# Performance work log

Measured on AMD Instinct MI355X. Metric: run time of the kernel, lower is better.

Reference implementation:

```python
import jax, jax.numpy as jnp
import numpy as np

B, T, C = 64, 384, 256
NH, NKV = 4, 2
HD = C // NH            # 64
NREP = NH // NKV        # 2
NE, TOPK = 8, 2
HID = int(8 / 3 * C)    # 682
EPS_RMS = 1e-6


def _rope_tables(t_len):
    inv_freq = 1.0 / (10000.0 ** (np.arange(0, HD, 2, dtype=np.float32) / HD))
    t = np.arange(t_len, dtype=np.float32)
    freqs = np.outer(t, inv_freq)                      # [T, HD/2]
    emb = np.concatenate([freqs, freqs], axis=-1)      # [T, HD]
    return jnp.asarray(np.cos(emb)), jnp.asarray(np.sin(emb))


def _rotate_half(x):
    h = x.shape[-1] // 2
    return jnp.concatenate([-x[..., h:], x[..., :h]], axis=-1)


def _rmsnorm(v, w):
    return v * jax.lax.rsqrt(jnp.mean(v * v, axis=-1, keepdims=True) + EPS_RMS) * w


def setup_inputs() -> dict:
    key = jax.random.key(0)
    ks = jax.random.split(key, 10)
    s = lambda k, shape: (jax.random.normal(k, shape, jnp.float32) * 0.02)
    return {
        "x": jax.random.normal(ks[0], (B, T, C), jnp.float32),
        "ln1_w": jnp.ones((C,), jnp.float32),
        "ln2_w": jnp.ones((C,), jnp.float32),
        "wq": s(ks[1], (NH * HD, C)),
        "wk": s(ks[2], (NKV * HD, C)),
        "wv": s(ks[3], (NKV * HD, C)),
        "wo": s(ks[4], (C, C)),
        "router_w": s(ks[5], (NE, C)),
        "w1": s(ks[6], (NE, HID, C)),
        "w2": s(ks[7], (NE, C, HID)),
        "w3": s(ks[8], (NE, HID, C)),
    }


def reference(x, ln1_w, ln2_w, wq, wk, wv, wo, router_w, w1, w2, w3):
    Bx, Tx, Cx = x.shape
    # --- attention sub-block ---
    h = _rmsnorm(x, ln1_w)
    q = (h @ wq.T).reshape(Bx, Tx, NH, HD).transpose(0, 2, 1, 3)    # [B,H,T,D]
    k = (h @ wk.T).reshape(Bx, Tx, NKV, HD).transpose(0, 2, 1, 3)   # [B,KV,T,D]
    v = (h @ wv.T).reshape(Bx, Tx, NKV, HD).transpose(0, 2, 1, 3)
    cos, sin = _rope_tables(Tx)
    cos, sin = cos[None, None], sin[None, None]
    q = q * cos + _rotate_half(q) * sin
    k = k * cos + _rotate_half(k) * sin
    k = jnp.repeat(k, NREP, axis=1)   # GQA: expand kv heads
    v = jnp.repeat(v, NREP, axis=1)
    scores = jnp.einsum('bhtd,bhsd->bhts', q, k) / jnp.sqrt(jnp.float32(HD))
    causal = jnp.tril(jnp.ones((Tx, Tx), dtype=bool))
    scores = jnp.where(causal[None, None], scores, jnp.float32(-1e30))
    att = jax.nn.softmax(scores, axis=-1)
    y = jnp.einsum('bhts,bhsd->bhtd', att, v).transpose(0, 2, 1, 3).reshape(Bx, Tx, Cx)
    x = x + y @ wo.T

    # --- MoE sub-block ---
    flat = _rmsnorm(x, ln2_w).reshape(-1, Cx)                  # [N, C]
    probs = jax.nn.softmax(flat @ router_w.T, axis=-1)         # [N, NE]
    tp, ti = jax.lax.top_k(probs, TOPK)
    tp = tp / (jnp.sum(tp, axis=-1, keepdims=True) + 1e-9)
    # per-token per-expert combine weight (0 if not selected)
    weights = jnp.sum(tp[..., None] * jax.nn.one_hot(ti, NE, dtype=flat.dtype), axis=1)  # [N, NE]
    out = jnp.zeros_like(flat)
    for e in range(NE):  # small fixed expert count
        hh = jax.nn.silu(flat @ w1[e].T) * (flat @ w3[e].T)
        out = out + weights[:, e:e + 1] * (hh @ w2[e].T)
    return x + out.reshape(Bx, Tx, Cx)
```

## Files before the change

### kernel.cpp

```cpp
#include <hip/hip_runtime.h>
#include <hip/hip_bf16.h>
#include <math.h>

typedef unsigned short u16t;
typedef __bf16 bf16x8 __attribute__((ext_vector_type(8)));
typedef float f32x4 __attribute__((ext_vector_type(4)));

#define NBATCH 64
#define NT 384
#define NC 256
#define NHID 682
#define NHIDP 704
#define NTOK (NBATCH * NT)
#define NSLOT (2 * NTOK + 1024)

static __device__ __forceinline__ float bf2f(u16t u) { return __uint_as_float(((unsigned int)u) << 16); }
static __device__ __forceinline__ u16t f2bf(float f) { return __builtin_bit_cast(u16t, __float2bfloat16(f)); }

static __device__ __forceinline__ void gload16(const void* gp, void* lp) {
  __builtin_amdgcn_global_load_lds((const __attribute__((address_space(1))) void*)gp,
                                   (__attribute__((address_space(3))) void*)lp, 16, 0, 0);
}


__global__ void k_cvt(const float* __restrict__ src, u16t* __restrict__ dst, int n) {
  int i = blockIdx.x * 256 + threadIdx.x;
  if (i < n) dst[i] = f2bf(src[i]);
}

__global__ __launch_bounds__(256) void k_rms(const float* __restrict__ xin,
                                             const float* __restrict__ wg,
                                             u16t* __restrict__ out) {
  int w = threadIdx.x >> 6, l = threadIdx.x & 63;
  int n = blockIdx.x * 4 + w;
  const float* xr = xin + (size_t)n * NC;
  float4 xa = *(const float4*)(xr + l * 4);
  float ssq = xa.x * xa.x + xa.y * xa.y + xa.z * xa.z + xa.w * xa.w;
  for (int d = 1; d < 64; d <<= 1) ssq += __shfl_xor(ssq, d, 64);
  float rs = rsqrtf(ssq * (1.f / 256.f) + 1e-6f);
  float4 wa = *(const float4*)(wg + l * 4);
  ushort4 o;
  o.x = f2bf(xa.x * rs * wa.x);
  o.y = f2bf(xa.y * rs * wa.y);
  o.z = f2bf(xa.z * rs * wa.z);
  o.w = f2bf(xa.w * rs * wa.w);
  *(ushort4*)(out + (size_t)n * NC + l * 4) = o;
}

__global__ __launch_bounds__(256) void k_rms_router(const float* __restrict__ xin,
                                                    const float* __restrict__ wg,
                                                    const float* __restrict__ rw,
                                                    u16t* __restrict__ flat,
                                                    int* __restrict__ eidx,
                                                    float* __restrict__ ew) {
  int w = threadIdx.x >> 6, l = threadIdx.x & 63;
  int n = blockIdx.x * 4 + w;
  const float* xr = xin + (size_t)n * NC;
  float4 xa = *(const float4*)(xr + l * 4);
  float ssq = xa.x * xa.x + xa.y * xa.y + xa.z * xa.z + xa.w * xa.w;
  for (int d = 1; d < 64; d <<= 1) ssq += __shfl_xor(ssq, d, 64);
  float rs = rsqrtf(ssq * (1.f / 256.f) + 1e-6f);
  float4 wa = *(const float4*)(wg + l * 4);
  float n0 = xa.x * rs * wa.x, n1 = xa.y * rs * wa.y;
  float n2 = xa.z * rs * wa.z, n3 = xa.w * rs * wa.w;
  ushort4 o; o.x = f2bf(n0); o.y = f2bf(n1); o.z = f2bf(n2); o.w = f2bf(n3);
  *(ushort4*)(flat + (size_t)n * NC + l * 4) = o;
  float acc[8];
  for (int e = 0; e < 8; e++) {
    float4 ra = *(const float4*)(rw + (size_t)e * NC + l * 4);
    acc[e] = n0 * ra.x + n1 * ra.y + n2 * ra.z + n3 * ra.w;
  }
  for (int e = 0; e < 8; e++)
    for (int d = 1; d < 64; d <<= 1) acc[e] += __shfl_xor(acc[e], d, 64);
  if (l == 0) {
    float mx = acc[0];
    for (int e = 1; e < 8; e++) mx = fmaxf(mx, acc[e]);
    float p[8], sum = 0.f;
    for (int e = 0; e < 8; e++) { p[e] = __expf(acc[e] - mx); sum += p[e]; }
    float inv = 1.f / sum;
    for (int e = 0; e < 8; e++) p[e] *= inv;
    int i0 = 0; float b0 = p[0];
    for (int e = 1; e < 8; e++) if (p[e] > b0) { b0 = p[e]; i0 = e; }
    int i1 = -1; float b1 = -1.f;
    for (int e = 0; e < 8; e++) if (e != i0 && p[e] > b1) { b1 = p[e]; i1 = e; }
    float s2 = 1.f / (b0 + b1 + 1e-9f);
    eidx[n * 2] = i0; eidx[n * 2 + 1] = i1;
    ew[n * 2] = b0 * s2; ew[n * 2 + 1] = b1 * s2;
  }
}

__global__ __launch_bounds__(256) void k_hist(const int* __restrict__ eidx, int* __restrict__ cnt) {
  __shared__ int lh[8];
  if (threadIdx.x < 8) lh[threadIdx.x] = 0;
  __syncthreads();
  int base = blockIdx.x * 1024 + threadIdx.x;
  for (int i = 0; i < 4; i++) atomicAdd(&lh[eidx[base + i * 256]], 1);
  __syncthreads();
  if (threadIdx.x < 8) atomicAdd(&cnt[threadIdx.x], lh[threadIdx.x]);
}

__global__ __launch_bounds__(256) void k_gemm_bt(const u16t* __restrict__ A,
                                                 const u16t* __restrict__ Bw,
                                                 u16t* __restrict__ Co, int K, int N) {
  __shared__ __align__(16) u16t sA[128 * 64];
  __shared__ __align__(16) u16t sB[128 * 64];
  int t = threadIdx.x;
  int m0 = blockIdx.y * 128, n0 = blockIdx.x * 128;
  int w = t >> 6, l = t & 63, quad = l >> 4, lq = l & 15;
  int wm = (w >> 1) * 64, wn = (w & 1) * 64;
  const f32x4 fz = {0.f, 0.f, 0.f, 0.f};
  f32x4 acc[4][4];
  for (int i = 0; i < 4; i++) for (int j = 0; j < 4; j++) acc[i][j] = fz;
  int nk = K >> 6;
  for (int kb = 0; kb < nk; kb++) {
    int k0 = kb << 6;
    for (int i = 0; i < 4; i++) {
      int c = i * 256 + t; int r = c >> 3; int g = (c & 7) ^ (r & 7);
      gload16(A + (size_t)(m0 + r) * K + k0 + g * 8, sA + (size_t)c * 8);
      gload16(Bw + (size_t)(n0 + r) * K + k0 + g * 8, sB + (size_t)c * 8);
    }
    __syncthreads();
    for (int kk = 0; kk < 2; kk++) {
      int gq = kk * 4 + quad;
      bf16x8 af[4], bf[4];
      for (int mi = 0; mi < 4; mi++) { int row = wm + mi * 16 + lq; af[mi] = *(const bf16x8*)(sA + (row * 8 + (gq ^ (row & 7))) * 8); }
      for (int ni = 0; ni < 4; ni++) { int row = wn + ni * 16 + lq; bf[ni] = *(const bf16x8*)(sB + (row * 8 + (gq ^ (row & 7))) * 8); }
      for (int mi = 0; mi < 4; mi++)
        for (int ni = 0; ni < 4; ni++)
          acc[mi][ni] = __builtin_amdgcn_mfma_f32_16x16x32_bf16(af[mi], bf[ni], acc[mi][ni], 0, 0, 0);
    }
    __syncthreads();
  }
  for (int mi = 0; mi < 4; mi++)
    for (int ni = 0; ni < 4; ni++) {
      int gn = n0 + wn + ni * 16 + lq;
      for (int r = 0; r < 4; r++) {
        int gm = m0 + wm + mi * 16 + quad * 4 + r;
        Co[(size_t)gm * N + gn] = f2bf(acc[mi][ni][r]);
      }
    }
}

__global__ __launch_bounds__(256) void k_gemm_wo(const u16t* __restrict__ A,
                                                 const u16t* __restrict__ Bw,
                                                 const float* __restrict__ xin,
                                                 float* __restrict__ xo) {
  __shared__ __align__(16) u16t sA[128 * 64];
  __shared__ __align__(16) u16t sB[128 * 64];
  int t = threadIdx.x;
  int m0 = blockIdx.y * 128, n0 = blockIdx.x * 128;
  int w = t >> 6, l = t & 63, quad = l >> 4, lq = l & 15;
  int wm = (w >> 1) * 64, wn = (w & 1) * 64;
  const f32x4 fz = {0.f, 0.f, 0.f, 0.f};
  f32x4 acc[4][4];
  for (int i = 0; i < 4; i++) for (int j = 0; j < 4; j++) acc[i][j] = fz;
  for (int kb = 0; kb < 4; kb++) {
    int k0 = kb << 6;
    for (int i = 0; i < 4; i++) {
      int c = i * 256 + t; int r = c >> 3; int g = (c & 7) ^ (r & 7);
      gload16(A + (size_t)(m0 + r) * NC + k0 + g * 8, sA + (size_t)c * 8);
      gload16(Bw + (size_t)(n0 + r) * NC + k0 + g * 8, sB + (size_t)c * 8);
    }
    __syncthreads();
    for (int kk = 0; kk < 2; kk++) {
      int gq = kk * 4 + quad;
      bf16x8 af[4], bf[4];
      for (int mi = 0; mi < 4; mi++) { int row = wm + mi * 16 + lq; af[mi] = *(const bf16x8*)(sA + (row * 8 + (gq ^ (row & 7))) * 8); }
      for (int ni = 0; ni < 4; ni++) { int row = wn + ni * 16 + lq; bf[ni] = *(const bf16x8*)(sB + (row * 8 + (gq ^ (row & 7))) * 8); }
      for (int mi = 0; mi < 4; mi++)
        for (int ni = 0; ni < 4; ni++)
          acc[mi][ni] = __builtin_amdgcn_mfma_f32_16x16x32_bf16(af[mi], bf[ni], acc[mi][ni], 0, 0, 0);
    }
    __syncthreads();
  }
  for (int mi = 0; mi < 4; mi++)
    for (int ni = 0; ni < 4; ni++) {
      int gn = n0 + wn + ni * 16 + lq;
      for (int r = 0; r < 4; r++) {
        int gm = m0 + wm + mi * 16 + quad * 4 + r;
        xo[(size_t)gm * NC + gn] = acc[mi][ni][r] + xin[(size_t)gm * NC + gn];
      }
    }
}

__global__ __launch_bounds__(192) void k_rope(u16t* __restrict__ q, u16t* __restrict__ kbuf) {
  int n = blockIdx.x; int t = n % NT;
  int i = threadIdx.x;
  u16t* base; int d;
  if (i < 128) { base = q + (size_t)n * NC + (i >> 5) * 64; d = i & 31; }
  else { int j = i - 128; base = kbuf + (size_t)n * 128 + (j >> 5) * 64; d = j & 31; }
  float x1 = bf2f(base[d]), x2 = bf2f(base[d + 32]);
  float ang = (float)t * powf(10000.f, -(float)d * (1.f / 32.f));
  float s, c; sincosf(ang, &s, &c);
  base[d] = f2bf(x1 * c - x2 * s);
  base[d + 32] = f2bf(x2 * c + x1 * s);
}

__global__ __launch_bounds__(256) void k_attn(const u16t* __restrict__ q,
                                              const u16t* __restrict__ kbuf,
                                              const u16t* __restrict__ vbuf,
                                              u16t* __restrict__ y) {
  __shared__ __align__(16) u16t sK[64 * 64];
  __shared__ __align__(16) u16t sVT[64 * 64];
  __shared__ __align__(16) u16t sP[4 * 32 * 64];
  int qt = blockIdx.x, h = blockIdx.y, b = blockIdx.z;
  int kvh = h >> 1;
  int t = threadIdx.x, w = t >> 6, l = t & 63, quad = l >> 4, lq = l & 15;
  int tb = qt * 128 + w * 32;
  bf16x8 qf[2][2];
  for (int mi = 0; mi < 2; mi++)
    for (int kk = 0; kk < 2; kk++)
      qf[mi][kk] = *(const bf16x8*)(q + ((size_t)(b * NT + tb + mi * 16 + lq)) * NC + h * 64 + kk * 32 + quad * 8);
  const f32x4 fz = {0.f, 0.f, 0.f, 0.f};
  f32x4 accO[2][4];
  float mrow[2][4], lrow[2][4];
  for (int mi = 0; mi < 2; mi++)
    for (int ni = 0; ni < 4; ni++) accO[mi][ni] = fz;
  for (int mi = 0; mi < 2; mi++)
    for (int r = 0; r < 4; r++) { mrow[mi][r] = -1e30f; lrow[mi][r] = 0.f; }
  u16t* myP = sP + w * 2048;
  int nkt = (qt + 1) * 2;
  for (int kt = 0; kt < nkt; kt++) {
    int s0 = kt * 64;
    for (int i = 0; i < 2; i++) {
      int c = i * 256 + t; int s = c >> 3; int g = (c & 7) ^ (s & 7);
      gload16(kbuf + ((size_t)(b * NT + s0 + s)) * 128 + kvh * 64 + g * 8, sK + (size_t)c * 8);
    }
    for (int i = 0; i < 2; i++) {
      int p = i * 256 + t; int n0g = p >> 6; int s = p & 63; int n0 = n0g * 8;
      const u16t* vp = vbuf + ((size_t)(b * NT + s0 + s)) * 128 + kvh * 64 + n0;
      ushort4 v0 = *(const ushort4*)vp; ushort4 v1 = *(const ushort4*)(vp + 4);
      u16t vv[8] = {v0.x, v0.y, v0.z, v0.w, v1.x, v1.y, v1.z, v1.w};
      for (int j = 0; j < 8; j++) {
        int nn = n0 + j;
        sVT[(nn * 8 + ((s >> 3) ^ (nn & 7))) * 8 + (s & 7)] = vv[j];
      }
    }
    __syncthreads();
    if (s0 <= tb + 31) {
      f32x4 accS[2][4];
      for (int mi = 0; mi < 2; mi++) for (int ni = 0; ni < 4; ni++) accS[mi][ni] = fz;
      for (int kk = 0; kk < 2; kk++) {
        int gq = kk * 4 + quad;
        bf16x8 kf[4];
        for (int ni = 0; ni < 4; ni++) { int row = ni * 16 + lq; kf[ni] = *(const bf16x8*)(sK + (row * 8 + (gq ^ (row & 7))) * 8); }
        for (int mi = 0; mi < 2; mi++)
          for (int ni = 0; ni < 4; ni++)
            accS[mi][ni] = __builtin_amdgcn_mfma_f32_16x16x32_bf16(qf[mi][kk], kf[ni], accS[mi][ni], 0, 0, 0);
      }
      for (int mi = 0; mi < 2; mi++) {
        float alpha[4];
        for (int r = 0; r < 4; r++) {
          int trow = tb + mi * 16 + quad * 4 + r;
          float mx = -1e30f;
          for (int ni = 0; ni < 4; ni++) {
            int ss = s0 + ni * 16 + lq;
            float sv = accS[mi][ni][r] * 0.125f;
            sv = (ss > trow) ? -1e30f : sv;
            accS[mi][ni][r] = sv;
            mx = fmaxf(mx, sv);
          }
          for (int d = 1; d < 16; d <<= 1) mx = fmaxf(mx, __shfl_xor(mx, d, 64));
          float mnew = fmaxf(mrow[mi][r], mx);
          float al = __expf(mrow[mi][r] - mnew);
          float rsum = 0.f;
          for (int ni = 0; ni < 4; ni++) {
            float p = __expf(accS[mi][ni][r] - mnew);
            accS[mi][ni][r] = p;
            rsum += p;
          }
          for (int d = 1; d < 16; d <<= 1) rsum += __shfl_xor(rsum, d, 64);
          lrow[mi][r] = lrow[mi][r] * al + rsum;
          mrow[mi][r] = mnew;
          alpha[r] = al;
        }
        for (int ni = 0; ni < 4; ni++)
          for (int r = 0; r < 4; r++) accO[mi][ni][r] *= alpha[r];
        for (int ni = 0; ni < 4; ni++) {
          int cc = ni * 16 + lq;
          for (int r = 0; r < 4; r++) {
            int row = mi * 16 + quad * 4 + r;
            myP[((cc >> 3) * 32 + row) * 8 + (cc & 7)] = f2bf(accS[mi][ni][r]);
          }
        }
      }
      asm volatile("s_waitcnt lgkmcnt(0)" ::: "memory");
      for (int kk = 0; kk < 2; kk++) {
        int gq = kk * 4 + quad;
        bf16x8 pf[2], vf[4];
        for (int mi = 0; mi < 2; mi++) { int row = mi * 16 + lq; pf[mi] = *(const bf16x8*)(myP + (gq * 32 + row) * 8); }
        for (int ni = 0; ni < 4; ni++) { int row = ni * 16 + lq; vf[ni] = *(const bf16x8*)(sVT + (row * 8 + (gq ^ (row & 7))) * 8); }
        for (int mi = 0; mi < 2; mi++)
          for (int ni = 0; ni < 4; ni++)
            accO[mi][ni] = __builtin_amdgcn_mfma_f32_16x16x32_bf16(pf[mi], vf[ni], accO[mi][ni], 0, 0, 0);
      }
    }
    __syncthreads();
  }
  for (int mi = 0; mi < 2; mi++)
    for (int r = 0; r < 4; r++) {
      int trow = tb + mi * 16 + quad * 4 + r;
      float inv = 1.f / lrow[mi][r];
      for (int ni = 0; ni < 4; ni++) {
        int d = ni * 16 + lq;
        y[((size_t)(b * NT + trow)) * NC + h * 64 + d] = f2bf(accO[mi][ni][r] * inv);
      }
    }
}

__global__ void k_init(int* __restrict__ tok, float* __restrict__ tokw, int* __restrict__ ctrl) {
  int i = blockIdx.x * 256 + threadIdx.x;
  if (i < NSLOT) { tok[i] = -1; tokw[i] = 0.f; }
  if (blockIdx.x == 0 && threadIdx.x < 64) ctrl[threadIdx.x] = 0;
}

__global__ void k_scan(const int* __restrict__ cnt, int* __restrict__ offs, int* __restrict__ cursor) {
  if (threadIdx.x == 0) {
    int off = 0;
    for (int e = 0; e < 8; e++) {
      offs[e] = off; cursor[e] = off;
      off += ((cnt[e] + 127) >> 7) << 7;
    }
    offs[8] = off;
  }
}

__global__ __launch_bounds__(256) void k_scatter(const int* __restrict__ eidx, const float* __restrict__ ew,
                                                 int* __restrict__ cursor, int* __restrict__ tok,
                                                 float* __restrict__ tokw, int* __restrict__ t2s) {
  __shared__ int lcnt[8], lbase[8];
  if (threadIdx.x < 8) lcnt[threadIdx.x] = 0;
  __syncthreads();
  int n = blockIdx.x * 256 + threadIdx.x;
  int e0 = eidx[n * 2], e1 = eidx[n * 2 + 1];
  int p0 = atomicAdd(&lcnt[e0], 1);
  int p1 = atomicAdd(&lcnt[e1], 1);
  __syncthreads();
  if (threadIdx.x < 8) lbase[threadIdx.x] = atomicAdd(&cursor[threadIdx.x], lcnt[threadIdx.x]);
  __syncthreads();
  int g0 = lbase[e0] + p0, g1 = lbase[e1] + p1;
  tok[g0] = n; tokw[g0] = ew[n * 2];
  tok[g1] = n; tokw[g1] = ew[n * 2 + 1];
  t2s[n * 2] = g0; t2s[n * 2 + 1] = g1;
}

__global__ void k_pack13(const float* __restrict__ w1, const float* __restrict__ w3,
                         u16t* __restrict__ w1p, u16t* __restrict__ w3p) {
  int idx = blockIdx.x * 256 + threadIdx.x;
  int kcol = idx & 255; int tmp = idx >> 8; int nrow = tmp % NHIDP; int e = tmp / NHIDP;
  if (nrow < NHID) {
    size_t src = ((size_t)e * NHID + nrow) * NC + kcol;
    w1p[idx] = f2bf(w1[src]); w3p[idx] = f2bf(w3[src]);
  } else { w1p[idx] = 0; w3p[idx] = 0; }
}

__global__ void k_pack2(const float* __restrict__ w2, u16t* __restrict__ w2p) {
  int idx = blockIdx.x * 256 + threadIdx.x;
  int kcol = idx % NHIDP; int tmp = idx / NHIDP; int nrow = tmp & 255; int e = tmp >> 8;
  w2p[idx] = (kcol < NHID) ? f2bf(w2[((size_t)e * NC + nrow) * NHID + kcol]) : (u16t)0;
}

__global__ __launch_bounds__(256) void k_moe_e1(const u16t* __restrict__ flat,
                                                const u16t* __restrict__ w1p,
                                                const u16t* __restrict__ w3p,
                                                const int* __restrict__ offs,
                                                const int* __restrict__ tok,
                                                u16t* __restrict__ hh) {
  __shared__ __align__(16) u16t sA[128 * 64];
  __shared__ __align__(16) u16t sB1[64 * 64];
  __shared__ __align__(16) u16t sB3[64 * 64];
  int t = threadIdx.x;
  int bid = blockIdx.x;
  int work = (bid & 7) * 539 + (bid >> 3);
  int sb = work / 11;
  int slot0 = sb * 128, n0 = (work - sb * 11) * 64;
  int e = 7;
  for (int i = 0; i < 8; i++) { if (slot0 < offs[i + 1]) { e = i; break; } }
  const u16t* B1 = w1p + (size_t)e * NHIDP * NC;
  const u16t* B3 = w3p + (size_t)e * NHIDP * NC;
  int w = t >> 6, l = t & 63, quad = l >> 4, lq = l & 15;
  int wm = (w >> 1) * 64, wn = (w & 1) * 32;
  const f32x4 fz = {0.f, 0.f, 0.f, 0.f};
  f32x4 a1[4][2], a3[4][2];
  for (int i = 0; i < 4; i++) for (int j = 0; j < 2; j++) { a1[i][j] = fz; a3[i][j] = fz; }
  for (int kb = 0; kb < 4; kb++) {
    int k0 = kb << 6;
    for (int i = 0; i < 4; i++) {
      int c = i * 256 + t; int r = c >> 3; int g = (c & 7) ^ (r & 7);
      int tk = tok[slot0 + r]; int row = (tk < 0) ? 0 : tk;
      gload16(flat + (size_t)row * NC + k0 + g * 8, sA + (size_t)c * 8);
    }
    for (int i = 0; i < 2; i++) {
      int c = i * 256 + t; int r = c >> 3; int g = (c & 7) ^ (r & 7);
      gload16(B1 + (size_t)(n0 + r) * NC + k0 + g * 8, sB1 + (size_t)c * 8);
      gload16(B3 + (size_t)(n0 + r) * NC + k0 + g * 8, sB3 + (size_t)c * 8);
    }
    __syncthreads();
    for (int kk = 0; kk < 2; kk++) {
      int gq = kk * 4 + quad;
      bf16x8 af[4], b1f[2], b3f[2];
      for (int mi = 0; mi < 4; mi++) { int row = wm + mi * 16 + lq; af[mi] = *(const bf16x8*)(sA + (row * 8 + (gq ^ (row & 7))) * 8); }
      for (int ni = 0; ni < 2; ni++) {
        int row = wn + ni * 16 + lq;
        b1f[ni] = *(const bf16x8*)(sB1 + (row * 8 + (gq ^ (row & 7))) * 8);
        b3f[ni] = *(const bf16x8*)(sB3 + (row * 8 + (gq ^ (row & 7))) * 8);
      }
      for (int mi = 0; mi < 4; mi++)
        for (int ni = 0; ni < 2; ni++) {
          a1[mi][ni] = __builtin_amdgcn_mfma_f32_16x16x32_bf16(af[mi], b1f[ni], a1[mi][ni], 0, 0, 0);
          a3[mi][ni] = __builtin_amdgcn_mfma_f32_16x16x32_bf16(af[mi], b3f[ni], a3[mi][ni], 0, 0, 0);
        }
    }
    __syncthreads();
  }
  for (int mi = 0; mi < 4; mi++)
    for (int ni = 0; ni < 2; ni++) {
      int gn = n0 + wn + ni * 16 + lq;
      for (int r = 0; r < 4; r++) {
        int slot = slot0 + wm + mi * 16 + quad * 4 + r;
        float v1 = a1[mi][ni][r], v3 = a3[mi][ni][r];
        float hv = v1 / (1.f + __expf(-v1)) * v3;
        hh[(size_t)slot * NHIDP + gn] = f2bf(hv);
      }
    }
}

__global__ __launch_bounds__(256) void k_moe_e2(const u16t* __restrict__ hh,
                                                const u16t* __restrict__ w2p,
                                                const int* __restrict__ offs,
                                                const float* __restrict__ tokw,
                                                u16t* __restrict__ eo) {
  __shared__ __align__(16) u16t sA[128 * 64];
  __shared__ __align__(16) u16t sB[128 * 64];
  int t = threadIdx.x;
  int bid = blockIdx.x;
  int work = (bid & 7) * 98 + (bid >> 3);
  int slot0 = (work >> 1) * 128, n0 = (work & 1) * 128;
  int e = 7;
  for (int i = 0; i < 8; i++) { if (slot0 < offs[i + 1]) { e = i; break; } }
  const u16t* Bw = w2p + (size_t)e * NC * NHIDP;
  int w = t >> 6, l = t & 63, quad = l >> 4, lq = l & 15;
  int wm = (w >> 1) * 64, wn = (w & 1) * 64;
  const f32x4 fz = {0.f, 0.f, 0.f, 0.f};
  f32x4 acc[4][4];
  for (int i = 0; i < 4; i++) for (int j = 0; j < 4; j++) acc[i][j] = fz;
  for (int kb = 0; kb < 11; kb++) {
    int k0 = kb << 6;
    for (int i = 0; i < 4; i++) {
      int c = i * 256 + t; int r = c >> 3; int g = (c & 7) ^ (r & 7);
      gload16(hh + (size_t)(slot0 + r) * NHIDP + k0 + g * 8, sA + (size_t)c * 8);
      gload16(Bw + (size_t)(n0 + r) * NHIDP + k0 + g * 8, sB + (size_t)c * 8);
    }
    __syncthreads();
    for (int kk = 0; kk < 2; kk++) {
      int gq = kk * 4 + quad;
      bf16x8 af[4], bf[4];
      for (int mi = 0; mi < 4; mi++) { int row = wm + mi * 16 + lq; af[mi] = *(const bf16x8*)(sA + (row * 8 + (gq ^ (row & 7))) * 8); }
      for (int ni = 0; ni < 4; ni++) { int row = wn + ni * 16 + lq; bf[ni] = *(const bf16x8*)(sB + (row * 8 + (gq ^ (row & 7))) * 8); }
      for (int mi = 0; mi < 4; mi++)
        for (int ni = 0; ni < 4; ni++)
          acc[mi][ni] = __builtin_amdgcn_mfma_f32_16x16x32_bf16(af[mi], bf[ni], acc[mi][ni], 0, 0, 0);
    }
    __syncthreads();
  }
  for (int mi = 0; mi < 4; mi++)
    for (int r = 0; r < 4; r++) {
      int slot = slot0 + wm + mi * 16 + quad * 4 + r;
      float wgt = tokw[slot];
      for (int ni = 0; ni < 4; ni++) {
        int gn = n0 + wn + ni * 16 + lq;
        eo[(size_t)slot * NC + gn] = f2bf(wgt * acc[mi][ni][r]);
      }
    }
}

__global__ __launch_bounds__(256) void k_combine(const u16t* __restrict__ eo,
                                                 const int* __restrict__ t2s,
                                                 float* __restrict__ xo) {
  int w = threadIdx.x >> 6, l = threadIdx.x & 63;
  int n = blockIdx.x * 4 + w;
  int g0 = t2s[n * 2], g1 = t2s[n * 2 + 1];
  float* xr = xo + (size_t)n * NC + l * 4;
  float4 xa = *(const float4*)xr;
  ushort4 a = *(const ushort4*)(eo + (size_t)g0 * NC + l * 4);
  ushort4 b = *(const ushort4*)(eo + (size_t)g1 * NC + l * 4);
  xa.x += bf2f(a.x) + bf2f(b.x);
  xa.y += bf2f(a.y) + bf2f(b.y);
  xa.z += bf2f(a.z) + bf2f(b.z);
  xa.w += bf2f(a.w) + bf2f(b.w);
  *(float4*)xr = xa;
}

extern "C" void kernel_launch(void* const* d_in, const int* in_sizes, int n_in,
                              void* d_out, int out_size, void* d_ws, size_t ws_size,
                              hipStream_t stream) {
  (void)in_sizes; (void)n_in; (void)out_size; (void)ws_size;
  const float* x    = (const float*)d_in[0];
  const float* ln1w = (const float*)d_in[1];
  const float* ln2w = (const float*)d_in[2];
  const float* wq   = (const float*)d_in[3];
  const float* wk   = (const float*)d_in[4];
  const float* wv   = (const float*)d_in[5];
  const float* wo   = (const float*)d_in[6];
  const float* rw   = (const float*)d_in[7];
  const float* w1   = (const float*)d_in[8];
  const float* w2   = (const float*)d_in[9];
  const float* w3   = (const float*)d_in[10];
  float* xo = (float*)d_out;

  char* ws = (char*)d_ws;
  size_t off = 0;
  int* ctrl  = (int*)(ws + off);  off += 4096;
  int* eidx  = (int*)(ws + off);  off += (size_t)NTOK * 2 * 4;
  float* ew  = (float*)(ws + off); off += (size_t)NTOK * 2 * 4;
  int* tok   = (int*)(ws + off);  off += (size_t)NSLOT * 4;
  float* tokw = (float*)(ws + off); off += (size_t)NSLOT * 4;
  int* t2s   = (int*)(ws + off);  off += (size_t)NTOK * 2 * 4;
  u16t* wqb  = (u16t*)(ws + off); off += (size_t)256 * 256 * 2;
  u16t* wkb  = (u16t*)(ws + off); off += (size_t)128 * 256 * 2;
  u16t* wvb  = (u16t*)(ws + off); off += (size_t)128 * 256 * 2;
  u16t* wob  = (u16t*)(ws + off); off += (size_t)256 * 256 * 2;
  u16t* w1p  = (u16t*)(ws + off); off += (size_t)8 * NHIDP * NC * 2;
  u16t* w3p  = (u16t*)(ws + off); off += (size_t)8 * NHIDP * NC * 2;
  u16t* w2p  = (u16t*)(ws + off); off += (size_t)8 * NC * NHIDP * 2;
  u16t* h    = (u16t*)(ws + off); off += (size_t)NTOK * NC * 2;
  u16t* q    = (u16t*)(ws + off); off += (size_t)NTOK * NC * 2;
  u16t* kbuf = (u16t*)(ws + off); off += (size_t)NTOK * 128 * 2;
  u16t* vbuf = (u16t*)(ws + off); off += (size_t)NTOK * 128 * 2;
  u16t* y    = (u16t*)(ws + off); off += (size_t)NTOK * NC * 2;
  u16t* flat = (u16t*)(ws + off); off += (size_t)NTOK * NC * 2;
  u16t* hh   = (u16t*)(ws + off); off += (size_t)NSLOT * NHIDP * 2;
  u16t* eo   = h;
  int* cnt = ctrl; int* offs = ctrl + 8; int* cursor = ctrl + 20;

  k_init<<<NSLOT / 256, 256, 0, stream>>>(tok, tokw, ctrl);
  k_cvt<<<256, 256, 0, stream>>>(wq, wqb, 65536);
  k_cvt<<<128, 256, 0, stream>>>(wk, wkb, 32768);
  k_cvt<<<128, 256, 0, stream>>>(wv, wvb, 32768);
  k_cvt<<<256, 256, 0, stream>>>(wo, wob, 65536);
  k_pack13<<<(8 * NHIDP * NC) / 256, 256, 0, stream>>>(w1, w3, w1p, w3p);
  k_pack2<<<(8 * NC * NHIDP) / 256, 256, 0, stream>>>(w2, w2p);

  k_rms<<<NTOK / 4, 256, 0, stream>>>(x, ln1w, h);
  k_gemm_bt<<<dim3(2, NTOK / 128), 256, 0, stream>>>(h, wqb, q, NC, 256);
  k_gemm_bt<<<dim3(1, NTOK / 128), 256, 0, stream>>>(h, wkb, kbuf, NC, 128);
  k_gemm_bt<<<dim3(1, NTOK / 128), 256, 0, stream>>>(h, wvb, vbuf, NC, 128);
  k_rope<<<NTOK, 192, 0, stream>>>(q, kbuf);
  k_attn<<<dim3(3, 4, NBATCH), 256, 0, stream>>>(q, kbuf, vbuf, y);
  k_gemm_wo<<<dim3(2, NTOK / 128), 256, 0, stream>>>(y, wob, x, xo);

  k_rms_router<<<NTOK / 4, 256, 0, stream>>>(xo, ln2w, rw, flat, eidx, ew);
  k_hist<<<48, 256, 0, stream>>>(eidx, cnt);
  k_scan<<<1, 64, 0, stream>>>(cnt, offs, cursor);
  k_scatter<<<NTOK / 256, 256, 0, stream>>>(eidx, ew, cursor, tok, tokw, t2s);
  k_moe_e1<<<4312, 256, 0, stream>>>(flat, w1p, w3p, offs, tok, hh);
  k_moe_e2<<<784, 256, 0, stream>>>(hh, w2p, offs, tokw, eo);
  k_combine<<<NTOK / 4, 256, 0, stream>>>(eo, t2s, xo);
}
```

Before: 347.8 us.

## Fuse setup kernels, merge QKV GEMM with RoPE epilogue, fold scan into hist

All the weight-conversion, packing and init kernels become one multi-role setup kernel, which also precomputes a RoPE cos/sin table. The three Q/K/V GEMMs become a single GEMM writing an interleaved qkv buffer, with RoPE applied in its epilogue, so the separate rope kernel and its extra read-modify-write pass over q and k go away. The scan is folded into the histogram kernel through a last-block-done atomic counter. GEMM address arithmetic is also hoisted out of the k-loops. The goal is fewer launches and less memory traffic, at the cost of more complex fused kernels and reliance on atomic fence ordering for the scan.

Result: faster. 312.2 us (-10.2%).

```diff
diff --git a/kernel.cpp b/kernel.cpp
--- a/kernel.cpp
+++ b/kernel.cpp
@@ -14,6 +14,13 @@
 #define NTOK (NBATCH * NT)
 #define NSLOT (2 * NTOK + 1024)
 
+#define SB0 196
+#define SB1 (SB0 + 512)
+#define SB2 (SB1 + 256)
+#define SB3 (SB2 + 5632)
+#define SB4 (SB3 + 5632)
+#define SB5 (SB4 + 48)
+
 static __device__ __forceinline__ float bf2f(u16t u) { return __uint_as_float(((unsigned int)u) << 16); }
 static __device__ __forceinline__ u16t f2bf(float f) { return __builtin_bit_cast(u16t, __float2bfloat16(f)); }
 
@@ -23,9 +30,48 @@
 }
 
 
-__global__ void k_cvt(const float* __restrict__ src, u16t* __restrict__ dst, int n) {
-  int i = blockIdx.x * 256 + threadIdx.x;
-  if (i < n) dst[i] = f2bf(src[i]);
+__global__ __launch_bounds__(256) void k_setup(const float* __restrict__ wq, const float* __restrict__ wk,
+                                               const float* __restrict__ wv, const float* __restrict__ wo,
+                                               const float* __restrict__ w1, const float* __restrict__ w2,
+                                               const float* __restrict__ w3,
+                                               int* __restrict__ tok, float* __restrict__ tokw,
+                                               int* __restrict__ ctrl,
+                                               u16t* __restrict__ wqkvb, u16t* __restrict__ wob,
+                                               u16t* __restrict__ w1p, u16t* __restrict__ w3p,
+                                               u16t* __restrict__ w2p, float* __restrict__ rtab) {
+  int blk = blockIdx.x, t = threadIdx.x;
+  if (blk < SB0) {
+    int i = blk * 256 + t;
+    tok[i] = -1; tokw[i] = 0.f;
+    if (blk == 0 && t < 64) ctrl[t] = 0;
+  } else if (blk < SB1) {
+    int i = (blk - SB0) * 256 + t;
+    int row = i >> 8, col = i & 255;
+    float s = (row < 256) ? wq[(size_t)row * 256 + col]
+            : (row < 384) ? wk[(size_t)(row - 256) * 256 + col]
+                          : wv[(size_t)(row - 384) * 256 + col];
+    wqkvb[i] = f2bf(s);
+  } else if (blk < SB2) {
+    int i = (blk - SB1) * 256 + t;
+    wob[i] = f2bf(wo[i]);
+  } else if (blk < SB3) {
+    int idx = (blk - SB2) * 256 + t;
+    int kcol = idx & 255; int tmp = idx >> 8; int nrow = tmp % NHIDP; int e = tmp / NHIDP;
+    if (nrow < NHID) {
+      size_t src = ((size_t)e * NHID + nrow) * NC + kcol;
+      w1p[idx] = f2bf(w1[src]); w3p[idx] = f2bf(w3[src]);
+    } else { w1p[idx] = 0; w3p[idx] = 0; }
+  } else if (blk < SB4) {
+    int idx = (blk - SB3) * 256 + t;
+    int kcol = idx % NHIDP; int tmp = idx / NHIDP; int nrow = tmp & 255; int e = tmp >> 8;
+    w2p[idx] = (kcol < NHID) ? f2bf(w2[((size_t)e * NC + nrow) * NHID + kcol]) : (u16t)0;
+  } else {
+    int i = (blk - SB4) * 256 + t;
+    int tt = i >> 5, d = i & 31;
+    float ang = (float)tt * powf(10000.f, -(float)d * (1.f / 32.f));
+    float s, c; sincosf(ang, &s, &c);
+    ((float2*)rtab)[i] = make_float2(c, s);
+  }
 }
 
 __global__ __launch_bounds__(256) void k_rms(const float* __restrict__ xin,
@@ -89,35 +135,57 @@
   }
 }
 
-__global__ __launch_bounds__(256) void k_hist(const int* __restrict__ eidx, int* __restrict__ cnt) {
+__global__ __launch_bounds__(256) void k_hist(const int* __restrict__ eidx, int* __restrict__ ctrl) {
+  int* cnt = ctrl; int* offs = ctrl + 8; int* cursor = ctrl + 20; int* done = ctrl + 32;
   __shared__ int lh[8];
   if (threadIdx.x < 8) lh[threadIdx.x] = 0;
   __syncthreads();
   int base = blockIdx.x * 1024 + threadIdx.x;
   for (int i = 0; i < 4; i++) atomicAdd(&lh[eidx[base + i * 256]], 1);
   __syncthreads();
-  if (threadIdx.x < 8) atomicAdd(&cnt[threadIdx.x], lh[threadIdx.x]);
-}
-
-__global__ __launch_bounds__(256) void k_gemm_bt(const u16t* __restrict__ A,
-                                                 const u16t* __restrict__ Bw,
-                                                 u16t* __restrict__ Co, int K, int N) {
+  if (threadIdx.x < 8) {
+    atomicAdd(&cnt[threadIdx.x], lh[threadIdx.x]);
+    __threadfence();
+  }
+  __syncthreads();
+  if (threadIdx.x == 0) {
+    int prev = atomicAdd(done, 1);
+    if (prev == 47) {
+      int off = 0;
+      for (int e = 0; e < 8; e++) {
+        int c_ = atomicAdd(&cnt[e], 0);
+        offs[e] = off; cursor[e] = off;
+        off += ((c_ + 127) >> 7) << 7;
+      }
+      offs[8] = off;
+    }
+  }
+}
+
+__global__ __launch_bounds__(256) void k_gemm_qkv(const u16t* __restrict__ A,
+                                                  const u16t* __restrict__ Bw,
+                                                  const float* __restrict__ rtab,
+                                                  u16t* __restrict__ qkv) {
   __shared__ __align__(16) u16t sA[128 * 64];
   __shared__ __align__(16) u16t sB[128 * 64];
   int t = threadIdx.x;
   int m0 = blockIdx.y * 128, n0 = blockIdx.x * 128;
   int w = t >> 6, l = t & 63, quad = l >> 4, lq = l & 15;
   int wm = (w >> 1) * 64, wn = (w & 1) * 64;
+  const u16t* aP[4]; const u16t* bP[4];
+  for (int i = 0; i < 4; i++) {
+    int c = i * 256 + t; int r = c >> 3; int g = (c & 7) ^ (r & 7);
+    aP[i] = A + (size_t)(m0 + r) * NC + g * 8;
+    bP[i] = Bw + (size_t)(n0 + r) * NC + g * 8;
+  }
   const f32x4 fz = {0.f, 0.f, 0.f, 0.f};
   f32x4 acc[4][4];
   for (int i = 0; i < 4; i++) for (int j = 0; j < 4; j++) acc[i][j] = fz;
-  int nk = K >> 6;
-  for (int kb = 0; kb < nk; kb++) {
+  for (int kb = 0; kb < 4; kb++) {
     int k0 = kb << 6;
     for (int i = 0; i < 4; i++) {
-      int c = i * 256 + t; int r = c >> 3; int g = (c & 7) ^ (r & 7);
-      gload16(A + (size_t)(m0 + r) * K + k0 + g * 8, sA + (size_t)c * 8);
-      gload16(Bw + (size_t)(n0 + r) * K + k0 + g * 8, sB + (size_t)c * 8);
+      gload16(aP[i] + k0, sA + (size_t)(i * 256 + t) * 8);
+      gload16(bP[i] + k0, sB + (size_t)(i * 256 + t) * 8);
     }
     __syncthreads();
     for (int kk = 0; kk < 2; kk++) {
@@ -131,12 +199,23 @@
     }
     __syncthreads();
   }
+  int cb = (n0 + wn) >> 6;
+  const float2* rt = (const float2*)rtab;
   for (int mi = 0; mi < 4; mi++)
-    for (int ni = 0; ni < 4; ni++) {
-      int gn = n0 + wn + ni * 16 + lq;
-      for (int r = 0; r < 4; r++) {
-        int gm = m0 + wm + mi * 16 + quad * 4 + r;
-        Co[(size_t)gm * N + gn] = f2bf(acc[mi][ni][r]);
+    for (int r = 0; r < 4; r++) {
+      int gm = m0 + wm + mi * 16 + quad * 4 + r;
+      u16t* orow = qkv + (size_t)gm * 512 + n0 + wn;
+      if (cb < 6) {
+        int tt = gm % NT;
+        for (int ni = 0; ni < 2; ni++) {
+          int d = ni * 16 + lq;
+          float2 cs = rt[tt * 32 + d];
+          float x1 = acc[mi][ni][r], x2 = acc[mi][ni + 2][r];
+          orow[d] = f2bf(x1 * cs.x - x2 * cs.y);
+          orow[d + 32] = f2bf(x2 * cs.x + x1 * cs.y);
+        }
+      } else {
+        for (int ni = 0; ni < 4; ni++) orow[ni * 16 + lq] = f2bf(acc[mi][ni][r]);
       }
     }
 }
@@ -151,15 +230,20 @@
   int m0 = blockIdx.y * 128, n0 = blockIdx.x * 128;
   int w = t >> 6, l = t & 63, quad = l >> 4, lq = l & 15;
   int wm = (w >> 1) * 64, wn = (w & 1) * 64;
+  const u16t* aP[4]; const u16t* bP[4];
+  for (int i = 0; i < 4; i++) {
+    int c = i * 256 + t; int r = c >> 3; int g = (c & 7) ^ (r & 7);
+    aP[i] = A + (size_t)(m0 + r) * NC + g * 8;
+    bP[i] = Bw + (size_t)(n0 + r) * NC + g * 8;
+  }
   const f32x4 fz = {0.f, 0.f, 0.f, 0.f};
   f32x4 acc[4][4];
   for (int i = 0; i < 4; i++) for (int j = 0; j < 4; j++) acc[i][j] = fz;
   for (int kb = 0; kb < 4; kb++) {
     int k0 = kb << 6;
     for (int i = 0; i < 4; i++) {
-      int c = i * 256 + t; int r = c >> 3; int g = (c & 7) ^ (r & 7);
-      gload16(A + (size_t)(m0 + r) * NC + k0 + g * 8, sA + (size_t)c * 8);
-      gload16(Bw + (size_t)(n0 + r) * NC + k0 + g * 8, sB + (size_t)c * 8);
+      gload16(aP[i] + k0, sA + (size_t)(i * 256 + t) * 8);
+      gload16(bP[i] + k0, sB + (size_t)(i * 256 + t) * 8);
     }
     __syncthreads();
     for (int kk = 0; kk < 2; kk++) {
@@ -183,22 +267,7 @@
     }
 }
 
-__global__ __launch_bounds__(192) void k_rope(u16t* __restrict__ q, u16t* __restrict__ kbuf) {
-  int n = blockIdx.x; int t = n % NT;
-  int i = threadIdx.x;
-  u16t* base; int d;
-  if (i < 128) { base = q + (size_t)n * NC + (i >> 5) * 64; d = i & 31; }
-  else { int j = i - 128; base = kbuf + (size_t)n * 128 + (j >> 5) * 64; d = j & 31; }
-  float x1 = bf2f(base[d]), x2 = bf2f(base[d + 32]);
-  float ang = (float)t * powf(10000.f, -(float)d * (1.f / 32.f));
-  float s, c; sincosf(ang, &s, &c);
-  base[d] = f2bf(x1 * c - x2 * s);
-  base[d + 32] = f2bf(x2 * c + x1 * s);
-}
-
-__global__ __launch_bounds__(256) void k_attn(const u16t* __restrict__ q,
-                                              const u16t* __restrict__ kbuf,
-                                              const u16t* __restrict__ vbuf,
+__global__ __launch_bounds__(256) void k_attn(const u16t* __restrict__ qkv,
                                               u16t* __restrict__ y) {
   __shared__ __align__(16) u16t sK[64 * 64];
   __shared__ __align__(16) u16t sVT[64 * 64];
@@ -210,7 +279,7 @@
   bf16x8 qf[2][2];
   for (int mi = 0; mi < 2; mi++)
     for (int kk = 0; kk < 2; kk++)
-      qf[mi][kk] = *(const bf16x8*)(q + ((size_t)(b * NT + tb + mi * 16 + lq)) * NC + h * 64 + kk * 32 + quad * 8);
+      qf[mi][kk] = *(const bf16x8*)(qkv + ((size_t)(b * NT + tb + mi * 16 + lq)) * 512 + h * 64 + kk * 32 + quad * 8);
   const f32x4 fz = {0.f, 0.f, 0.f, 0.f};
   f32x4 accO[2][4];
   float mrow[2][4], lrow[2][4];
@@ -224,11 +293,11 @@
     int s0 = kt * 64;
     for (int i = 0; i < 2; i++) {
       int c = i * 256 + t; int s = c >> 3; int g = (c & 7) ^ (s & 7);
-      gload16(kbuf + ((size_t)(b * NT + s0 + s)) * 128 + kvh * 64 + g * 8, sK + (size_t)c * 8);
+      gload16(qkv + ((size_t)(b * NT + s0 + s)) * 512 + 256 + kvh * 64 + g * 8, sK + (size_t)c * 8);
     }
     for (int i = 0; i < 2; i++) {
       int p = i * 256 + t; int n0g = p >> 6; int s = p & 63; int n0 = n0g * 8;
-      const u16t* vp = vbuf + ((size_t)(b * NT + s0 + s)) * 128 + kvh * 64 + n0;
+      const u16t* vp = qkv + ((size_t)(b * NT + s0 + s)) * 512 + 384 + kvh * 64 + n0;
       ushort4 v0 = *(const ushort4*)vp; ushort4 v1 = *(const ushort4*)(vp + 4);
       u16t vv[8] = {v0.x, v0.y, v0.z, v0.w, v1.x, v1.y, v1.z, v1.w};
       for (int j = 0; j < 8; j++) {
@@ -308,23 +377,6 @@
     }
 }
 
-__global__ void k_init(int* __restrict__ tok, float* __restrict__ tokw, int* __restrict__ ctrl) {
-  int i = blockIdx.x * 256 + threadIdx.x;
-  if (i < NSLOT) { tok[i] = -1; tokw[i] = 0.f; }
-  if (blockIdx.x == 0 && threadIdx.x < 64) ctrl[threadIdx.x] = 0;
-}
-
-__global__ void k_scan(const int* __restrict__ cnt, int* __restrict__ offs, int* __restrict__ cursor) {
-  if (threadIdx.x == 0) {
-    int off = 0;
-    for (int e = 0; e < 8; e++) {
-      offs[e] = off; cursor[e] = off;
-      off += ((cnt[e] + 127) >> 7) << 7;
-    }
-    offs[8] = off;
-  }
-}
-
 __global__ __launch_bounds__(256) void k_scatter(const int* __restrict__ eidx, const float* __restrict__ ew,
                                                  int* __restrict__ cursor, int* __restrict__ tok,
                                                  float* __restrict__ tokw, int* __restrict__ t2s) {
@@ -342,22 +394,6 @@
   tok[g0] = n; tokw[g0] = ew[n * 2];
   tok[g1] = n; tokw[g1] = ew[n * 2 + 1];
   t2s[n * 2] = g0; t2s[n * 2 + 1] = g1;
-}
-
-__global__ void k_pack13(const float* __restrict__ w1, const float* __restrict__ w3,
-                         u16t* __restrict__ w1p, u16t* __restrict__ w3p) {
-  int idx = blockIdx.x * 256 + threadIdx.x;
-  int kcol = idx & 255; int tmp = idx >> 8; int nrow = tmp % NHIDP; int e = tmp / NHIDP;
-  if (nrow < NHID) {
-    size_t src = ((size_t)e * NHID + nrow) * NC + kcol;
-    w1p[idx] = f2bf(w1[src]); w3p[idx] = f2bf(w3[src]);
-  } else { w1p[idx] = 0; w3p[idx] = 0; }
-}
-
-__global__ void k_pack2(const float* __restrict__ w2, u16t* __restrict__ w2p) {
-  int idx = blockIdx.x * 256 + threadIdx.x;
-  int kcol = idx % NHIDP; int tmp = idx / NHIDP; int nrow = tmp & 255; int e = tmp >> 8;
-  w2p[idx] = (kcol < NHID) ? f2bf(w2[((size_t)e * NC + nrow) * NHID + kcol]) : (u16t)0;
 }
 
 __global__ __launch_bounds__(256) void k_moe_e1(const u16t* __restrict__ flat,
@@ -380,20 +416,27 @@
   const u16t* B3 = w3p + (size_t)e * NHIDP * NC;
   int w = t >> 6, l = t & 63, quad = l >> 4, lq = l & 15;
   int wm = (w >> 1) * 64, wn = (w & 1) * 32;
+  const u16t* aP[4]; const u16t* b1P[2]; const u16t* b3P[2];
+  for (int i = 0; i < 4; i++) {
+    int c = i * 256 + t; int r = c >> 3; int g = (c & 7) ^ (r & 7);
+    int tk = tok[slot0 + r]; int row = (tk < 0) ? 0 : tk;
+    aP[i] = flat + (size_t)row * NC + g * 8;
+  }
+  for (int i = 0; i < 2; i++) {
+    int c = i * 256 + t; int r = c >> 3; int g = (c & 7) ^ (r & 7);
+    b1P[i] = B1 + (size_t)(n0 + r) * NC + g * 8;
+    b3P[i] = B3 + (size_t)(n0 + r) * NC + g * 8;
+  }
   const f32x4 fz = {0.f, 0.f, 0.f, 0.f};
   f32x4 a1[4][2], a3[4][2];
   for (int i = 0; i < 4; i++) for (int j = 0; j < 2; j++) { a1[i][j] = fz; a3[i][j] = fz; }
   for (int kb = 0; kb < 4; kb++) {
     int k0 = kb << 6;
-    for (int i = 0; i < 4; i++) {
-      int c = i * 256 + t; int r = c >> 3; int g = (c & 7) ^ (r & 7);
-      int tk = tok[slot0 + r]; int row = (tk < 0) ? 0 : tk;
-      gload16(flat + (size_t)row * NC + k0 + g * 8, sA + (size_t)c * 8);
-    }
+    for (int i = 0; i < 4; i++)
+      gload16(aP[i] + k0, sA + (size_t)(i * 256 + t) * 8);
     for (int i = 0; i < 2; i++) {
-      int c = i * 256 + t; int r = c >> 3; int g = (c & 7) ^ (r & 7);
-      gload16(B1 + (size_t)(n0 + r) * NC + k0 + g * 8, sB1 + (size_t)c * 8);
-      gload16(B3 + (size_t)(n0 + r) * NC + k0 + g * 8, sB3 + (size_t)c * 8);
+      gload16(b1P[i] + k0, sB1 + (size_t)(i * 256 + t) * 8);
+      gload16(b3P[i] + k0, sB3 + (size_t)(i * 256 + t) * 8);
     }
     __syncthreads();
     for (int kk = 0; kk < 2; kk++) {
@@ -441,15 +484,20 @@
   const u16t* Bw = w2p + (size_t)e * NC * NHIDP;
   int w = t >> 6, l = t & 63, quad = l >> 4, lq = l & 15;
   int wm = (w >> 1) * 64, wn = (w & 1) * 64;
+  const u16t* aP[4]; const u16t* bP[4];
+  for (int i = 0; i < 4; i++) {
+    int c = i * 256 + t; int r = c >> 3; int g = (c & 7) ^ (r & 7);
+    aP[i] = hh + (size_t)(slot0 + r) * NHIDP + g * 8;
+    bP[i] = Bw + (size_t)(n0 + r) * NHIDP + g * 8;
+  }
   const f32x4 fz = {0.f, 0.f, 0.f, 0.f};
   f32x4 acc[4][4];
   for (int i = 0; i < 4; i++) for (int j = 0; j < 4; j++) acc[i][j] = fz;
   for (int kb = 0; kb < 11; kb++) {
     int k0 = kb << 6;
     for (int i = 0; i < 4; i++) {
-      int c = i * 256 + t; int r = c >> 3; int g = (c & 7) ^ (r & 7);
-      gload16(hh + (size_t)(slot0 + r) * NHIDP + k0 + g * 8, sA + (size_t)c * 8);
-      gload16(Bw + (size_t)(n0 + r) * NHIDP + k0 + g * 8, sB + (size_t)c * 8);
+      gload16(aP[i] + k0, sA + (size_t)(i * 256 + t) * 8);
+      gload16(bP[i] + k0, sB + (size_t)(i * 256 + t) * 8);
     }
     __syncthreads();
     for (int kk = 0; kk < 2; kk++) {
@@ -516,42 +564,29 @@
   int* tok   = (int*)(ws + off);  off += (size_t)NSLOT * 4;
   float* tokw = (float*)(ws + off); off += (size_t)NSLOT * 4;
   int* t2s   = (int*)(ws + off);  off += (size_t)NTOK * 2 * 4;
-  u16t* wqb  = (u16t*)(ws + off); off += (size_t)256 * 256 * 2;
-  u16t* wkb  = (u16t*)(ws + off); off += (size_t)128 * 256 * 2;
-  u16t* wvb  = (u16t*)(ws + off); off += (size_t)128 * 256 * 2;
+  u16t* wqkvb = (u16t*)(ws + off); off += (size_t)512 * 256 * 2;
   u16t* wob  = (u16t*)(ws + off); off += (size_t)256 * 256 * 2;
   u16t* w1p  = (u16t*)(ws + off); off += (size_t)8 * NHIDP * NC * 2;
   u16t* w3p  = (u16t*)(ws + off); off += (size_t)8 * NHIDP * NC * 2;
   u16t* w2p  = (u16t*)(ws + off); off += (size_t)8 * NC * NHIDP * 2;
+  float* rtab = (float*)(ws + off); off += (size_t)NT * 32 * 2 * 4;
   u16t* h    = (u16t*)(ws + off); off += (size_t)NTOK * NC * 2;
-  u16t* q    = (u16t*)(ws + off); off += (size_t)NTOK * NC * 2;
-  u16t* kbuf = (u16t*)(ws + off); off += (size_t)NTOK * 128 * 2;
-  u16t* vbuf = (u16t*)(ws + off); off += (size_t)NTOK * 128 * 2;
+  u16t* qkv  = (u16t*)(ws + off); off += (size_t)NTOK * 512 * 2;
   u16t* y    = (u16t*)(ws + off); off += (size_t)NTOK * NC * 2;
   u16t* flat = (u16t*)(ws + off); off += (size_t)NTOK * NC * 2;
   u16t* hh   = (u16t*)(ws + off); off += (size_t)NSLOT * NHIDP * 2;
   u16t* eo   = h;
-  int* cnt = ctrl; int* offs = ctrl + 8; int* cursor = ctrl + 20;
-
-  k_init<<<NSLOT / 256, 256, 0, stream>>>(tok, tokw, ctrl);
-  k_cvt<<<256, 256, 0, stream>>>(wq, wqb, 65536);
-  k_cvt<<<128, 256, 0, stream>>>(wk, wkb, 32768);
-  k_cvt<<<128, 256, 0, stream>>>(wv, wvb, 32768);
-  k_cvt<<<256, 256, 0, stream>>>(wo, wob, 65536);
-  k_pack13<<<(8 * NHIDP * NC) / 256, 256, 0, stream>>>(w1, w3, w1p, w3p);
-  k_pack2<<<(8 * NC * NHIDP) / 256, 256, 0, stream>>>(w2, w2p);
-
+  int* offs = ctrl + 8; int* cursor = ctrl + 20;
+
+  k_setup<<<SB5, 256, 0, stream>>>(wq, wk, wv, wo, w1, w2, w3,
+                                   tok, tokw, ctrl, wqkvb, wob, w1p, w3p, w2p, rtab);
   k_rms<<<NTOK / 4, 256, 0, stream>>>(x, ln1w, h);
-  k_gemm_bt<<<dim3(2, NTOK / 128), 256, 0, stream>>>(h, wqb, q, NC, 256);
-  k_gemm_bt<<<dim3(1, NTOK / 128), 256, 0, stream>>>(h, wkb, kbuf, NC, 128);
-  k_gemm_bt<<<dim3(1, NTOK / 128), 256, 0, stream>>>(h, wvb, vbuf, NC, 128);
-  k_rope<<<NTOK, 192, 0, stream>>>(q, kbuf);
-  k_attn<<<dim3(3, 4, NBATCH), 256, 0, stream>>>(q, kbuf, vbuf, y);
+  k_gemm_qkv<<<dim3(4, NTOK / 128), 256, 0, stream>>>(h, wqkvb, rtab, qkv);
+  k_attn<<<dim3(3, 4, NBATCH), 256, 0, stream>>>(qkv, y);
   k_gemm_wo<<<dim3(2, NTOK / 128), 256, 0, stream>>>(y, wob, x, xo);
 
   k_rms_router<<<NTOK / 4, 256, 0, stream>>>(xo, ln2w, rw, flat, eidx, ew);
-  k_hist<<<48, 256, 0, stream>>>(eidx, cnt);
-  k_scan<<<1, 64, 0, stream>>>(cnt, offs, cursor);
+  k_hist<<<48, 256, 0, stream>>>(eidx, ctrl);
   k_scatter<<<NTOK / 256, 256, 0, stream>>>(eidx, ew, cursor, tok, tokw, t2s);
   k_moe_e1<<<4312, 256, 0, stream>>>(flat, w1p, w3p, offs, tok, hh);
   k_moe_e2<<<784, 256, 0, stream>>>(hh, w2p, offs, tokw, eo);
```
